# Kernel tuning notes

Measured on AMD Instinct MI355X. Metric: run time of the kernel, lower is better.

The kernel has to match this reference:

```python
import jax, jax.numpy as jnp
import numpy as np

B, S, DIM, NHEADS = 2, 3072, 1536, 12
HEAD_DIM = DIM // NHEADS          # 128
C = HEAD_DIM // 2                 # 64, freq channels per position
GRID = (8, 16, 24)                # F,H,W with F*H*W == S (static per this config)
EPS = 1e-6
MAX_POS = 1024


def _rms(x, g):
    # RMSNorm over the full channel dim (applied BEFORE per-head reshape, as in Wan)
    y = jax.lax.rsqrt(jnp.mean(jnp.square(x), axis=-1, keepdims=True) + EPS)
    return x * y * g


def _rope_angles(freqs, grid):
    # Split the C freq channels over (F, H, W) axes: [C-2*(C//3), C//3, C//3]
    s1 = C // 3
    s0 = C - 2 * s1
    f, h, w = grid
    af = freqs[:f, :s0]                # [f, s0]
    ah = freqs[:h, s0:s0 + s1]         # [h, s1]
    aw = freqs[:w, s0 + s1:]           # [w, s1]
    ang = jnp.concatenate([
        jnp.broadcast_to(af[:, None, None, :], (f, h, w, s0)),
        jnp.broadcast_to(ah[None, :, None, :], (f, h, w, s1)),
        jnp.broadcast_to(aw[None, None, :, :], (f, h, w, s1)),
    ], axis=-1)
    return ang.reshape(f * h * w, 1, C)  # [S, 1, C]


def _rope(x, ang):
    # x: [B, S, N, D]; rotate interleaved (even, odd) pairs by angle (complex mult)
    b, s, n, d = x.shape
    xr = x.reshape(b, s, n, d // 2, 2)
    cos = jnp.cos(ang)[None]           # [1, S, 1, C]
    sin = jnp.sin(ang)[None]
    ye = xr[..., 0] * cos - xr[..., 1] * sin
    yo = xr[..., 0] * sin + xr[..., 1] * cos
    return jnp.stack([ye, yo], axis=-1).reshape(b, s, n, d)


def setup_inputs() -> dict:
    key = jax.random.key(0)
    ks = jax.random.split(key, 12)
    x = jax.random.normal(ks[0], (B, S, DIM), dtype=jnp.float32)
    seq_lens = jnp.full((B,), S, dtype=jnp.int32)
    grid_sizes = np.array([list(GRID)] * B, dtype=np.int32)
    # Rotary angles: pos * inv_freq per channel (precomputed table, as in Wan)
    inv = 1.0 / (10000.0 ** (np.arange(C, dtype=np.float32) / C))
    freqs = jnp.asarray(np.arange(MAX_POS, dtype=np.float32)[:, None] * inv[None, :])
    w = lambda k: jax.random.normal(k, (DIM, DIM), dtype=jnp.float32) * 0.02
    bz = lambda: jnp.zeros((DIM,), dtype=jnp.float32)
    return {
        "x": x, "seq_lens": seq_lens, "grid_sizes": grid_sizes, "freqs": freqs,
        "Wq": w(ks[1]), "bq": bz(), "Wk": w(ks[2]), "bk": bz(),
        "Wv": w(ks[3]), "bv": bz(), "Wo": w(ks[4]), "bo": bz(),
        "gq": jnp.ones((DIM,), dtype=jnp.float32),
        "gk": jnp.ones((DIM,), dtype=jnp.float32),
    }


def reference(x, seq_lens, grid_sizes, freqs, Wq, bq, Wk, bk, Wv, bv, Wo, bo, gq, gk):
    b, s, _ = x.shape
    # QKV projection + full-dim RMSNorm on q/k
    q = _rms(x @ Wq.T + bq, gq).reshape(b, s, NHEADS, HEAD_DIM)
    k = _rms(x @ Wk.T + bk, gk).reshape(b, s, NHEADS, HEAD_DIM)
    v = (x @ Wv.T + bv).reshape(b, s, NHEADS, HEAD_DIM)
    # 3D RoPE (grid is static; all samples share GRID)
    ang = _rope_angles(freqs, GRID)
    q = _rope(q, ang)
    k = _rope(k, ang)
    # full (non-causal) attention with key-length masking
    scale = 1.0 / np.sqrt(HEAD_DIM).astype(np.float32)
    scores = jnp.einsum('bsnd,btnd->bnst', q, k) * scale
    kmask = jnp.arange(s)[None, :] < seq_lens[:, None]          # [B, T]
    scores = jnp.where(kmask[:, None, None, :], scores, jnp.float32(-1e30))
    attn = jax.nn.softmax(scores, axis=-1)
    out = jnp.einsum('bnst,btnd->bsnd', attn, v).reshape(b, s, DIM)
    return out @ Wo.T + bo
```

## Files before the change

### kernel.cpp

```cpp
#include <hip/hip_runtime.h>
#include <hip/hip_bf16.h>
#include <stdint.h>

typedef __attribute__((ext_vector_type(8))) short short8;
typedef __attribute__((ext_vector_type(4))) float f32x4;
typedef __attribute__((ext_vector_type(16))) float f32x16;

constexpr int kDim   = 1536;
constexpr int kHeads = 12;
constexpr int kHd    = 128;
constexpr int kS     = 3072;
constexpr int kB     = 2;
constexpr int kQKV   = 3 * kDim;
constexpr float kEps   = 1e-6f;
constexpr float kQMul  = 0.08838834764831845f * 1.44269504089f;

__device__ __forceinline__ ushort f2bf(float f) {
    union { float f; uint32_t u; } c; c.f = f;
    uint32_t u = c.u;
    return (ushort)((u + 0x7fffu + ((u >> 16) & 1u)) >> 16);
}
__device__ __forceinline__ float bf2f(uint32_t h) {
    union { uint32_t u; float f; } c; c.u = h << 16;
    return c.f;
}
__device__ __forceinline__ void gload_lds16(const void* g, void* l) {
    __builtin_amdgcn_global_load_lds((const __attribute__((address_space(1))) void*)g,
                                     (__attribute__((address_space(3))) void*)l, 16, 0, 0);
}
__device__ __forceinline__ uint32_t cvtpk_bf16(float lo, float hi) {
    uint32_t r;
    asm("v_cvt_pk_bf16_f32 %0, %1, %2" : "=v"(r) : "v"(lo), "v"(hi));
    return r;
}

__global__ __launch_bounds__(256)
void cvt_kernel(const float* __restrict__ in, ushort* __restrict__ out, int n8)
{
    int i = blockIdx.x * 256 + threadIdx.x;
    if (i >= n8) return;
    const float4* p = (const float4*)in + (size_t)i * 2;
    float4 a = p[0], b = p[1];
    uint4 r;
    r.x = (uint32_t)f2bf(a.x) | ((uint32_t)f2bf(a.y) << 16);
    r.y = (uint32_t)f2bf(a.z) | ((uint32_t)f2bf(a.w) << 16);
    r.z = (uint32_t)f2bf(b.x) | ((uint32_t)f2bf(b.y) << 16);
    r.w = (uint32_t)f2bf(b.z) | ((uint32_t)f2bf(b.w) << 16);
    ((uint4*)out)[i] = r;
}

__global__ __launch_bounds__(256)
void cvt4_kernel(const float* __restrict__ s0, const float* __restrict__ s1,
                 const float* __restrict__ s2, const float* __restrict__ s3,
                 ushort* __restrict__ d0, ushort* __restrict__ d1,
                 ushort* __restrict__ d2, ushort* __restrict__ d3, int n8)
{
    int i = blockIdx.x * 256 + threadIdx.x;
    if (i >= n8) return;
    const float* in; ushort* out;
    switch (blockIdx.y) {
        case 0: in = s0; out = d0; break;
        case 1: in = s1; out = d1; break;
        case 2: in = s2; out = d2; break;
        default: in = s3; out = d3; break;
    }
    const float4* p = (const float4*)in + (size_t)i * 2;
    float4 a = p[0], b = p[1];
    uint4 r;
    r.x = (uint32_t)f2bf(a.x) | ((uint32_t)f2bf(a.y) << 16);
    r.y = (uint32_t)f2bf(a.z) | ((uint32_t)f2bf(a.w) << 16);
    r.z = (uint32_t)f2bf(b.x) | ((uint32_t)f2bf(b.y) << 16);
    r.w = (uint32_t)f2bf(b.z) | ((uint32_t)f2bf(b.w) << 16);
    ((uint4*)out)[i] = r;
}

__global__ __launch_bounds__(256)
void biascat_kernel(const float* __restrict__ bq, const float* __restrict__ bk,
                    const float* __restrict__ bv, float* __restrict__ out)
{
    int i = blockIdx.x * 256 + threadIdx.x;
    if (i >= kQKV) return;
    float v = (i < kDim) ? bq[i] : (i < 2*kDim) ? bk[i - kDim] : bv[i - 2*kDim];
    out[i] = v;
}

template<typename OutT>
__global__ __launch_bounds__(256)
void gemm_bf16(const ushort* __restrict__ A, const ushort* __restrict__ B,
               const float* __restrict__ bias, OutT* __restrict__ C,
               int M, int N, int K)
{
    __shared__ ushort As[128 * 32];
    __shared__ ushort Bs[128 * 32];
    const int t    = threadIdx.x;
    const int lane = t & 63;
    const int w    = t >> 6;
    const int wm = (w >> 1) * 64, wn = (w & 1) * 64;
    const int m0 = blockIdx.y * 128, n0 = blockIdx.x * 128;

    const int srow = t >> 2;
    const int skc  = (t & 3) * 8;
    const ushort* Ag = A + (size_t)(m0 + srow) * K + skc;
    const ushort* Bg = B + (size_t)(n0 + srow) * K + skc;
    const size_t half = (size_t)64 * K;

    f32x4 acc[4][4];
    #pragma unroll
    for (int m = 0; m < 4; ++m)
        #pragma unroll
        for (int n = 0; n < 4; ++n)
            #pragma unroll
            for (int i = 0; i < 4; ++i) acc[m][n][i] = 0.f;

    const int kk  = (lane >> 4) * 8;
    const int l15 = lane & 15;

    for (int k0 = 0; k0 < K; k0 += 32) {
        __syncthreads();
        gload_lds16(Ag + k0,        &As[t * 8]);
        gload_lds16(Ag + half + k0, &As[t * 8 + 2048]);
        gload_lds16(Bg + k0,        &Bs[t * 8]);
        gload_lds16(Bg + half + k0, &Bs[t * 8 + 2048]);
        __syncthreads();
        short8 af[4], bf[4];
        #pragma unroll
        for (int m = 0; m < 4; ++m) af[m] = *(const short8*)&As[(wm + m*16 + l15) * 32 + kk];
        #pragma unroll
        for (int n = 0; n < 4; ++n) bf[n] = *(const short8*)&Bs[(wn + n*16 + l15) * 32 + kk];
        #pragma unroll
        for (int m = 0; m < 4; ++m)
            #pragma unroll
            for (int n = 0; n < 4; ++n)
                acc[m][n] = __builtin_amdgcn_mfma_f32_16x16x32_bf16(af[m], bf[n], acc[m][n], 0, 0, 0);
    }

    const int r0 = (lane >> 4) * 4;
    #pragma unroll
    for (int m = 0; m < 4; ++m) {
        #pragma unroll
        for (int r = 0; r < 4; ++r) {
            const size_t row = (size_t)(m0 + wm + m*16 + r0 + r);
            #pragma unroll
            for (int n = 0; n < 4; ++n) {
                const int col = n0 + wn + n*16 + l15;
                float val = acc[m][n][r] + bias[col];
                if constexpr (sizeof(OutT) == 4) C[row * N + col] = val;
                else                             C[row * N + col] = f2bf(val);
            }
        }
    }
}

__global__ __launch_bounds__(256)
void vtrans_kernel(const ushort* __restrict__ qkv, ushort* __restrict__ vt)
{
    __shared__ ushort Ts[64][72];
    const int t  = threadIdx.x;
    const int s0 = blockIdx.x * 64;
    const int d0 = blockIdx.y * 64;
    const int bh = blockIdx.z;
    const int b = bh / kHeads, h = bh % kHeads;

    const int r = t >> 2, cc = (t & 3) * 16;
    const ushort* src = qkv + ((size_t)(b * kS) + s0 + r) * kQKV + 2*kDim + h * kHd + d0 + cc;
    uint4 a0 = *(const uint4*)src;
    uint4 a1 = *(const uint4*)(src + 8);
    *(uint4*)&Ts[r][cc]     = a0;
    *(uint4*)&Ts[r][cc + 8] = a1;
    __syncthreads();
    ushort tmp[16];
    #pragma unroll
    for (int j = 0; j < 16; ++j) tmp[j] = Ts[cc + j][r];
    ushort* dst = vt + ((size_t)(bh * kHd) + d0 + r) * kS + s0 + cc;
    *(uint4*)dst       = *(uint4*)&tmp[0];
    *(uint4*)(dst + 8) = *(uint4*)&tmp[8];
}

__global__ __launch_bounds__(192)
void rmsrope_kernel(ushort* __restrict__ qkv,
                    const float* __restrict__ gq, const float* __restrict__ gk,
                    const float* __restrict__ freqs, const int* __restrict__ grid_sizes)
{
    __shared__ float red[4];
    const int row   = blockIdx.x;
    const int which = blockIdx.y;
    ushort* ptr = qkv + (size_t)row * kQKV + which * kDim;
    const float* g = which ? gk : gq;
    const float outmul = which ? 1.0f : kQMul;
    const int t = threadIdx.x;

    uint4 raw = ((const uint4*)ptr)[t];
    float v[8];
    v[0] = bf2f(raw.x & 0xffff); v[1] = bf2f(raw.x >> 16);
    v[2] = bf2f(raw.y & 0xffff); v[3] = bf2f(raw.y >> 16);
    v[4] = bf2f(raw.z & 0xffff); v[5] = bf2f(raw.z >> 16);
    v[6] = bf2f(raw.w & 0xffff); v[7] = bf2f(raw.w >> 16);

    float ss = 0.f;
    #pragma unroll
    for (int i = 0; i < 8; ++i) ss += v[i] * v[i];
    #pragma unroll
    for (int off = 32; off >= 1; off >>= 1) ss += __shfl_xor(ss, off);
    if ((t & 63) == 0) red[t >> 6] = ss;
    __syncthreads();
    const float scale = rsqrtf((red[0] + red[1] + red[2]) * (1.f / kDim) + kEps);

    const int b = row / kS, s = row % kS;
    const int gh = grid_sizes[b*3 + 1], gw = grid_sizes[b*3 + 2];
    const int hw  = gh * gw;
    const int fi  = s / hw;
    const int rem = s - fi * hw;
    const int hi  = rem / gw;
    const int wi  = rem - hi * gw;

    const float4 g0 = *(const float4*)(g + t*8);
    const float4 g1 = *(const float4*)(g + t*8 + 4);
    const float gv[8] = {g0.x, g0.y, g0.z, g0.w, g1.x, g1.y, g1.z, g1.w};

    uint32_t out[4];
    #pragma unroll
    for (int jj = 0; jj < 4; ++jj) {
        const int p = t*4 + jj;
        const int c = p & 63;
        const int pos = (c < 22) ? fi : (c < 43 ? hi : wi);
        const float ang = freqs[pos * 64 + c];
        float sn, cs;
        sincosf(ang, &sn, &cs);
        const float e0 = v[2*jj]   * scale * gv[2*jj];
        const float e1 = v[2*jj+1] * scale * gv[2*jj+1];
        const float o0 = (e0 * cs - e1 * sn) * outmul;
        const float o1 = (e0 * sn + e1 * cs) * outmul;
        out[jj] = (uint32_t)f2bf(o0) | ((uint32_t)f2bf(o1) << 16);
    }
    uint4 ov; ov.x = out[0]; ov.y = out[1]; ov.z = out[2]; ov.w = out[3];
    ((uint4*)ptr)[t] = ov;
}

__global__ __launch_bounds__(256, 2)
void attn_kernel(const ushort* __restrict__ qkv, const ushort* __restrict__ vtb,
                 ushort* __restrict__ pA, ushort* __restrict__ pB,
                 float* __restrict__ ml, const int* __restrict__ seq_lens)
{
    __shared__ ushort Ks[64 * 128];
    __shared__ ushort VT[128 * 64];

    const int lin = blockIdx.x;
    const int L   = (lin & 7) * 144 + (lin >> 3);
    const int bh   = L / 48;
    const int rem  = L - bh * 48;
    const int half = rem / 24;
    const int qtile= rem - half * 24;
    const int h = bh % kHeads, b = bh / kHeads;
    const int seq = seq_lens[b];
    const int kbeg = half * (kS / 2);

    const int t = threadIdx.x, lane = t & 63, w = t >> 6;
    const int l31 = lane & 31, hi = lane >> 5;
    const int qrow = qtile * 128 + w * 32 + l31;

    const ushort* qbase = qkv + ((size_t)b * kS) * kQKV + h * kHd;
    const ushort* kbase = qkv + ((size_t)b * kS) * kQKV + kDim + h * kHd;
    const ushort* vtbase = vtb + ((size_t)(b * kHeads + h) * kHd) * kS;

    short8 qf[8];
    #pragma unroll
    for (int kb = 0; kb < 8; ++kb)
        qf[kb] = *(const short8*)(qbase + (size_t)qrow * kQKV + kb*16 + hi*8);

    f32x16 oacc[4];
    #pragma unroll
    for (int n = 0; n < 4; ++n)
        #pragma unroll
        for (int i = 0; i < 16; ++i) oacc[n][i] = 0.f;

    float m_run = -1e30f, l_run = 0.f;

    const int srow = t >> 4;
    const int scol = (t & 15) * 8;
    const int kl   = scol ^ ((srow & 7) << 3);
    const int vd0  = t >> 3;
    const int vscol = ((t & 7) * 8) ^ ((vd0 & 7) << 3);

    for (int kt = 0; kt < kS/2; kt += 64) {
        const int k0 = kbeg + kt;
        __syncthreads();
        #pragma unroll
        for (int c = 0; c < 4; ++c) {
            gload_lds16(kbase + (size_t)(k0 + srow + c*16) * kQKV + kl, &Ks[t*8 + c*2048]);
            gload_lds16(vtbase + (size_t)(vd0 + c*32) * kS + k0 + vscol, &VT[t*8 + c*2048]);
        }
        __syncthreads();

        f32x16 s0, s1;
        #pragma unroll
        for (int i = 0; i < 16; ++i) { s0[i] = 0.f; s1[i] = 0.f; }
        __builtin_amdgcn_s_setprio(1);
        #pragma unroll
        for (int kb = 0; kb < 8; ++kb) {
            const int col = (kb*16 + hi*8) ^ ((l31 & 7) << 3);
            short8 kf0 = *(const short8*)&Ks[l31 * 128 + col];
            short8 kf1 = *(const short8*)&Ks[(32 + l31) * 128 + col];
            s0 = __builtin_amdgcn_mfma_f32_32x32x16_bf16(kf0, qf[kb], s0, 0, 0, 0);
            s1 = __builtin_amdgcn_mfma_f32_32x32x16_bf16(kf1, qf[kb], s1, 0, 0, 0);
        }
        __builtin_amdgcn_s_setprio(0);

        float mx = -1e30f;
        if (k0 + 64 > seq) {
            #pragma unroll
            for (int r = 0; r < 16; ++r) {
                const int key = k0 + (r&3) + 8*(r>>2) + 4*hi;
                if (key >= seq)      s0[r] = -1e30f;
                if (key + 32 >= seq) s1[r] = -1e30f;
                mx = fmaxf(fmaxf(mx, s0[r]), s1[r]);
            }
        } else {
            #pragma unroll
            for (int r = 0; r < 16; ++r) mx = fmaxf(fmaxf(mx, s0[r]), s1[r]);
        }
        mx = fmaxf(mx, __shfl_xor(mx, 32));

        const bool skip = (mx <= m_run + 11.0f);
        if (!__all(skip)) {
            const float mnew = fmaxf(m_run, mx);
            const float alpha = exp2f(m_run - mnew);
            m_run = mnew;
            l_run *= alpha;
            #pragma unroll
            for (int r = 0; r < 16; ++r) {
                const float ar = __shfl(alpha, (r&3) + 8*(r>>2) + 4*hi);
                #pragma unroll
                for (int n = 0; n < 4; ++n) oacc[n][r] *= ar;
            }
        }

        float rs = 0.f;
        #pragma unroll
        for (int r = 0; r < 16; ++r) {
            s0[r] = exp2f(s0[r] - m_run);
            s1[r] = exp2f(s1[r] - m_run);
            rs += s0[r] + s1[r];
        }
        rs += __shfl_xor(rs, 32);
        l_run += rs;

        uint32_t u0[8], u1[8], w0[8], w1[8];
        #pragma unroll
        for (int i = 0; i < 8; ++i) {
            u0[i] = cvtpk_bf16(s0[2*i], s0[2*i+1]);
            u1[i] = cvtpk_bf16(s1[2*i], s1[2*i+1]);
        }
        #pragma unroll
        for (int i = 0; i < 8; ++i) {
            w0[i] = __shfl_xor(u0[i], 32);
            w1[i] = __shfl_xor(u1[i], 32);
        }
        union PF { uint32_t d[4]; short8 s8; };
        PF pa[4];
        pa[0].d[0] = hi ? w0[2] : u0[0];  pa[0].d[1] = hi ? w0[3] : u0[1];
        pa[0].d[2] = hi ? u0[2] : w0[0];  pa[0].d[3] = hi ? u0[3] : w0[1];
        pa[1].d[0] = hi ? w0[6] : u0[4];  pa[1].d[1] = hi ? w0[7] : u0[5];
        pa[1].d[2] = hi ? u0[6] : w0[4];  pa[1].d[3] = hi ? u0[7] : w0[5];
        pa[2].d[0] = hi ? w1[2] : u1[0];  pa[2].d[1] = hi ? w1[3] : u1[1];
        pa[2].d[2] = hi ? u1[2] : w1[0];  pa[2].d[3] = hi ? u1[3] : w1[1];
        pa[3].d[0] = hi ? w1[6] : u1[4];  pa[3].d[1] = hi ? w1[7] : u1[5];
        pa[3].d[2] = hi ? u1[6] : w1[4];  pa[3].d[3] = hi ? u1[7] : w1[5];

        __builtin_amdgcn_s_setprio(1);
        #pragma unroll
        for (int ks = 0; ks < 4; ++ks) {
            #pragma unroll
            for (int n = 0; n < 4; ++n) {
                const int d = n*32 + l31;
                const int colv = (ks*16 + hi*8) ^ ((l31 & 7) << 3);
                short8 vf = *(const short8*)&VT[d * 64 + colv];
                oacc[n] = __builtin_amdgcn_mfma_f32_32x32x16_bf16(pa[ks].s8, vf, oacc[n], 0, 0, 0);
            }
        }
        __builtin_amdgcn_s_setprio(0);
    }

    ushort* pOut = half ? pB : pA;
    const float linv = 1.f / l_run;
    #pragma unroll
    for (int r = 0; r < 16; ++r) {
        const int qr = (r&3) + 8*(r>>2) + 4*hi;
        const float lr = __shfl(linv, qr);
        const size_t row = (size_t)(b * kS) + qtile * 128 + w * 32 + qr;
        #pragma unroll
        for (int n = 0; n < 4; ++n)
            pOut[row * kDim + h * kHd + n*32 + l31] = f2bf(oacc[n][r] * lr);
    }
    if (lane < 32) {
        const int s = qtile * 128 + w * 32 + l31;
        const size_t idx = ((((size_t)(b * kHeads + h)) * 2 + half) * kS + s) * 2;
        ml[idx]     = m_run;
        ml[idx + 1] = l_run;
    }
}

__global__ __launch_bounds__(256)
void combine_kernel(const ushort* __restrict__ pA, const ushort* __restrict__ pB,
                    const float* __restrict__ ml, ushort* __restrict__ out, int n8)
{
    int i = blockIdx.x * 256 + threadIdx.x;
    if (i >= n8) return;
    const int row = i / 192;
    const int within = (i - row * 192) * 8;
    const int h = within >> 7;
    const int b = row / kS;
    const int s = row - b * kS;
    const size_t base = (((size_t)(b * kHeads + h)) * 2) * kS;
    const float m0 = ml[(base + s) * 2],        l0 = ml[(base + s) * 2 + 1];
    const float m1 = ml[(base + kS + s) * 2],   l1 = ml[(base + kS + s) * 2 + 1];
    const float m  = fmaxf(m0, m1);
    const float a0 = l0 * exp2f(m0 - m);
    const float a1 = l1 * exp2f(m1 - m);
    const float inv = 1.f / (a0 + a1);
    const float f0 = a0 * inv, f1 = a1 * inv;

    uint4 ua = ((const uint4*)pA)[i];
    uint4 ub = ((const uint4*)pB)[i];
    const uint32_t* da = (const uint32_t*)&ua;
    const uint32_t* db = (const uint32_t*)&ub;
    uint32_t rv[4];
    #pragma unroll
    for (int j = 0; j < 4; ++j) {
        float o0 = f0 * bf2f(da[j] & 0xffff) + f1 * bf2f(db[j] & 0xffff);
        float o1 = f0 * bf2f(da[j] >> 16)    + f1 * bf2f(db[j] >> 16);
        rv[j] = (uint32_t)f2bf(o0) | ((uint32_t)f2bf(o1) << 16);
    }
    uint4 r; r.x = rv[0]; r.y = rv[1]; r.z = rv[2]; r.w = rv[3];
    ((uint4*)out)[i] = r;
}

extern "C" void kernel_launch(void* const* d_in, const int* in_sizes, int n_in,
                              void* d_out, int out_size, void* d_ws, size_t ws_size,
                              hipStream_t stream)
{
    (void)in_sizes; (void)n_in; (void)out_size; (void)ws_size;
    const float* x          = (const float*)d_in[0];
    const int*   seq_lens   = (const int*)  d_in[1];
    const int*   grid_sizes = (const int*)  d_in[2];
    const float* freqs      = (const float*)d_in[3];
    const float* Wq = (const float*)d_in[4];
    const float* bq = (const float*)d_in[5];
    const float* Wk = (const float*)d_in[6];
    const float* bk = (const float*)d_in[7];
    const float* Wv = (const float*)d_in[8];
    const float* bv = (const float*)d_in[9];
    const float* Wo = (const float*)d_in[10];
    const float* bo = (const float*)d_in[11];
    const float* gq = (const float*)d_in[12];
    const float* gk = (const float*)d_in[13];
    float* out = (float*)d_out;

    const int M = kB * kS;
    const size_t szX = (size_t)M * kDim;
    const size_t szW = (size_t)kDim * kDim;

    ushort* xb   = (ushort*)d_ws;
    ushort* wqb  = xb   + szX;
    ushort* wkb  = wqb  + szW;
    ushort* wvb  = wkb  + szW;
    ushort* wob  = wvb  + szW;
    ushort* qkvb = wob  + szW;
    ushort* ab   = qkvb + 3*szX;
    ushort* vtb  = ab   + szX;
    ushort* pBuf = vtb  + szX;
    float*  biasqkv = (float*)(pBuf + szX);
    float*  ml   = biasqkv + kQKV;

    dim3 blk(256);
    cvt_kernel<<<dim3((int)(szX/8/256)), blk, 0, stream>>>(x, xb, (int)(szX/8));
    cvt4_kernel<<<dim3((int)(szW/8/256), 4), blk, 0, stream>>>(
        Wq, Wk, Wv, Wo, wqb, wkb, wvb, wob, (int)(szW/8));
    biascat_kernel<<<dim3(18), blk, 0, stream>>>(bq, bk, bv, biasqkv);

    gemm_bf16<ushort><<<dim3(kQKV/128, M/128), blk, 0, stream>>>(
        xb, wqb, biasqkv, qkvb, M, kQKV, kDim);

    rmsrope_kernel<<<dim3(M, 2), dim3(192), 0, stream>>>(qkvb, gq, gk, freqs, grid_sizes);
    vtrans_kernel<<<dim3(kS/64, 2, kB*kHeads), blk, 0, stream>>>(qkvb, vtb);

    attn_kernel<<<dim3(48 * kHeads * kB), blk, 0, stream>>>(
        qkvb, vtb, xb, pBuf, ml, seq_lens);
    combine_kernel<<<dim3((int)(szX/8/256)), blk, 0, stream>>>(
        xb, pBuf, ml, ab, (int)(szX/8));

    gemm_bf16<float><<<dim3(kDim/128, M/128), blk, 0, stream>>>(
        ab, wob, bo, out, M, kDim, kDim);
}
```

Baseline: 433.6 us.

## Double-buffer LDS tiles in bf16 GEMM with two-stage prefetch

The GEMM kernel now keeps two LDS buffers for the A and B tiles. It preloads the first two K-slices, then, after computing on one buffer, refills that buffer with slice j+2 while the other buffer is consumed. The goal is to hide global-to-LDS load latency behind MFMA work and to drop one barrier per K step. In exchange, LDS use doubles to 32KB per block, and correctness relies on the barrier draining the asynchronous LDS loads before the next buffer is read.

```diff
diff --git a/kernel.cpp b/kernel.cpp
--- a/kernel.cpp
+++ b/kernel.cpp
@@ -90,8 +90,8 @@
                const float* __restrict__ bias, OutT* __restrict__ C,
                int M, int N, int K)
 {
-    __shared__ ushort As[128 * 32];
-    __shared__ ushort Bs[128 * 32];
+    __shared__ ushort As[2][128 * 32];
+    __shared__ ushort Bs[2][128 * 32];
     const int t    = threadIdx.x;
     const int lane = t & 63;
     const int w    = t >> 6;
@@ -103,6 +103,7 @@
     const ushort* Ag = A + (size_t)(m0 + srow) * K + skc;
     const ushort* Bg = B + (size_t)(n0 + srow) * K + skc;
     const size_t half = (size_t)64 * K;
+    const int Nk = K / 32;
 
     f32x4 acc[4][4];
     #pragma unroll
@@ -115,23 +116,39 @@
     const int kk  = (lane >> 4) * 8;
     const int l15 = lane & 15;
 
-    for (int k0 = 0; k0 < K; k0 += 32) {
-        __syncthreads();
-        gload_lds16(Ag + k0,        &As[t * 8]);
-        gload_lds16(Ag + half + k0, &As[t * 8 + 2048]);
-        gload_lds16(Bg + k0,        &Bs[t * 8]);
-        gload_lds16(Bg + half + k0, &Bs[t * 8 + 2048]);
-        __syncthreads();
+    {
+        gload_lds16(Ag,            &As[0][t * 8]);
+        gload_lds16(Ag + half,     &As[0][t * 8 + 2048]);
+        gload_lds16(Bg,            &Bs[0][t * 8]);
+        gload_lds16(Bg + half,     &Bs[0][t * 8 + 2048]);
+        gload_lds16(Ag + 32,        &As[1][t * 8]);
+        gload_lds16(Ag + half + 32, &As[1][t * 8 + 2048]);
+        gload_lds16(Bg + 32,        &Bs[1][t * 8]);
+        gload_lds16(Bg + half + 32, &Bs[1][t * 8 + 2048]);
+    }
+    __syncthreads();
+
+    for (int j = 0; j < Nk; ++j) {
+        const int cur = j & 1;
         short8 af[4], bf[4];
         #pragma unroll
-        for (int m = 0; m < 4; ++m) af[m] = *(const short8*)&As[(wm + m*16 + l15) * 32 + kk];
-        #pragma unroll
-        for (int n = 0; n < 4; ++n) bf[n] = *(const short8*)&Bs[(wn + n*16 + l15) * 32 + kk];
+        for (int m = 0; m < 4; ++m) af[m] = *(const short8*)&As[cur][(wm + m*16 + l15) * 32 + kk];
+        #pragma unroll
+        for (int n = 0; n < 4; ++n) bf[n] = *(const short8*)&Bs[cur][(wn + n*16 + l15) * 32 + kk];
         #pragma unroll
         for (int m = 0; m < 4; ++m)
             #pragma unroll
             for (int n = 0; n < 4; ++n)
                 acc[m][n] = __builtin_amdgcn_mfma_f32_16x16x32_bf16(af[m], bf[n], acc[m][n], 0, 0, 0);
+
+        __syncthreads();
+        if (j + 2 < Nk) {
+            const int k2 = (j + 2) * 32;
+            gload_lds16(Ag + k2,        &As[cur][t * 8]);
+            gload_lds16(Ag + half + k2, &As[cur][t * 8 + 2048]);
+            gload_lds16(Bg + k2,        &Bs[cur][t * 8]);
+            gload_lds16(Bg + half + k2, &Bs[cur][t * 8 + 2048]);
+        }
     }
 
     const int r0 = (lane >> 4) * 4;
```

Measured after the change: 439.2 us. Within noise of the previous version (+1.3%).

## Split attention key tile into two 32-key halves to cut registers, raise occupancy

Applied to the files above, without the earlier changes.

The 64-key inner step is restructured into two sequential 32-key sub-steps, each doing QK^T, online softmax update and PV for its half, so only one 16-float score accumulator and half the P fragments are live at once. Launch bounds are raised from 2 to 3 blocks per SIMD-group target so the compiler aims for lower VGPR use and more resident waves. The trade-off is twice as many max/rescale/shuffle reductions per tile and shorter MFMA chains between softmax phases. Spills are possible if the new register budget is too tight.

```diff
diff --git a/kernel.cpp b/kernel.cpp
--- a/kernel.cpp
+++ b/kernel.cpp
@@ -236,7 +236,7 @@
     ((uint4*)ptr)[t] = ov;
 }
 
-__global__ __launch_bounds__(256, 2)
+__global__ __launch_bounds__(256, 3)
 void attn_kernel(const ushort* __restrict__ qkv, const ushort* __restrict__ vtb,
                  ushort* __restrict__ pA, ushort* __restrict__ pB,
                  float* __restrict__ ml, const int* __restrict__ seq_lens)
@@ -291,93 +291,84 @@
         }
         __syncthreads();
 
-        f32x16 s0, s1;
-        #pragma unroll
-        for (int i = 0; i < 16; ++i) { s0[i] = 0.f; s1[i] = 0.f; }
-        __builtin_amdgcn_s_setprio(1);
-        #pragma unroll
-        for (int kb = 0; kb < 8; ++kb) {
-            const int col = (kb*16 + hi*8) ^ ((l31 & 7) << 3);
-            short8 kf0 = *(const short8*)&Ks[l31 * 128 + col];
-            short8 kf1 = *(const short8*)&Ks[(32 + l31) * 128 + col];
-            s0 = __builtin_amdgcn_mfma_f32_32x32x16_bf16(kf0, qf[kb], s0, 0, 0, 0);
-            s1 = __builtin_amdgcn_mfma_f32_32x32x16_bf16(kf1, qf[kb], s1, 0, 0, 0);
+        #pragma unroll
+        for (int hb = 0; hb < 2; ++hb) {
+            f32x16 s;
+            #pragma unroll
+            for (int i = 0; i < 16; ++i) s[i] = 0.f;
+            __builtin_amdgcn_s_setprio(1);
+            #pragma unroll
+            for (int kb = 0; kb < 8; ++kb) {
+                const int col = (kb*16 + hi*8) ^ ((l31 & 7) << 3);
+                short8 kf = *(const short8*)&Ks[(hb*32 + l31) * 128 + col];
+                s = __builtin_amdgcn_mfma_f32_32x32x16_bf16(kf, qf[kb], s, 0, 0, 0);
+            }
+            __builtin_amdgcn_s_setprio(0);
+
+            const int kb0 = k0 + hb*32;
+            float mx = -1e30f;
+            if (kb0 + 32 > seq) {
+                #pragma unroll
+                for (int r = 0; r < 16; ++r) {
+                    if (kb0 + (r&3) + 8*(r>>2) + 4*hi >= seq) s[r] = -1e30f;
+                    mx = fmaxf(mx, s[r]);
+                }
+            } else {
+                #pragma unroll
+                for (int r = 0; r < 16; ++r) mx = fmaxf(mx, s[r]);
+            }
+            mx = fmaxf(mx, __shfl_xor(mx, 32));
+
+            const bool skip = (mx <= m_run + 11.0f);
+            if (!__all(skip)) {
+                const float mnew = fmaxf(m_run, mx);
+                const float alpha = exp2f(m_run - mnew);
+                m_run = mnew;
+                l_run *= alpha;
+                #pragma unroll
+                for (int r = 0; r < 16; ++r) {
+                    const float ar = __shfl(alpha, (r&3) + 8*(r>>2) + 4*hi);
+                    #pragma unroll
+                    for (int n = 0; n < 4; ++n) oacc[n][r] *= ar;
+                }
+            }
+
+            float rs = 0.f;
+            #pragma unroll
+            for (int r = 0; r < 16; ++r) {
+                s[r] = exp2f(s[r] - m_run);
+                rs += s[r];
+            }
+            rs += __shfl_xor(rs, 32);
+            l_run += rs;
+
+            uint32_t u[8], wv[8];
+            #pragma unroll
+            for (int i = 0; i < 8; ++i) u[i] = cvtpk_bf16(s[2*i], s[2*i+1]);
+            #pragma unroll
+            for (int i = 0; i < 8; ++i) wv[i] = __shfl_xor(u[i], 32);
+            union PF { uint32_t d[4]; short8 s8; };
+            PF pa0, pa1;
+            pa0.d[0] = hi ? wv[2] : u[0];  pa0.d[1] = hi ? wv[3] : u[1];
+            pa0.d[2] = hi ? u[2] : wv[0];  pa0.d[3] = hi ? u[3] : wv[1];
+            pa1.d[0] = hi ? wv[6] : u[4];  pa1.d[1] = hi ? wv[7] : u[5];
+            pa1.d[2] = hi ? u[6] : wv[4];  pa1.d[3] = hi ? u[7] : wv[5];
+
+            __builtin_amdgcn_s_setprio(1);
+            #pragma unroll
+            for (int kss = 0; kss < 2; ++kss) {
+                const int ks = hb*2 + kss;
+                #pragma unroll
+                for (int n = 0; n < 4; ++n) {
+                    const int d = n*32 + l31;
+                    const int colv = (ks*16 + hi*8) ^ ((l31 & 7) << 3);
+                    short8 vf = *(const short8*)&VT[d * 64 + colv];
+                    oacc[n] = __builtin_amdgcn_mfma_f32_32x32x16_bf16(
+                        (kss ? pa1 : pa0).s8, vf, oacc[n], 0, 0, 0);
+                }
+            }
+            __builtin_amdgcn_s_setprio(0);
         }
-        __builtin_amdgcn_s_setprio(0);
-
-        float mx = -1e30f;
-        if (k0 + 64 > seq) {
-            #pragma unroll
-            for (int r = 0; r < 16; ++r) {
-                const int key = k0 + (r&3) + 8*(r>>2) + 4*hi;
-                if (key >= seq)      s0[r] = -1e30f;
-                if (key + 32 >= seq) s1[r] = -1e30f;
-                mx = fmaxf(fmaxf(mx, s0[r]), s1[r]);
-            }
-        } else {
-            #pragma unroll
-            for (int r = 0; r < 16; ++r) mx = fmaxf(fmaxf(mx, s0[r]), s1[r]);
-        }
-        mx = fmaxf(mx, __shfl_xor(mx, 32));
-
-        const bool skip = (mx <= m_run + 11.0f);
-        if (!__all(skip)) {
-            const float mnew = fmaxf(m_run, mx);
-            const float alpha = exp2f(m_run - mnew);
-            m_run = mnew;
-            l_run *= alpha;
-            #pragma unroll
-            for (int r = 0; r < 16; ++r) {
-                const float ar = __shfl(alpha, (r&3) + 8*(r>>2) + 4*hi);
-                #pragma unroll
-                for (int n = 0; n < 4; ++n) oacc[n][r] *= ar;
-            }
-        }
-
-        float rs = 0.f;
-        #pragma unroll
-        for (int r = 0; r < 16; ++r) {
-            s0[r] = exp2f(s0[r] - m_run);
-            s1[r] = exp2f(s1[r] - m_run);
-            rs += s0[r] + s1[r];
-        }
-        rs += __shfl_xor(rs, 32);
-        l_run += rs;
-
-        uint32_t u0[8], u1[8], w0[8], w1[8];
-        #pragma unroll
-        for (int i = 0; i < 8; ++i) {
-            u0[i] = cvtpk_bf16(s0[2*i], s0[2*i+1]);
-            u1[i] = cvtpk_bf16(s1[2*i], s1[2*i+1]);
-        }
-        #pragma unroll
-        for (int i = 0; i < 8; ++i) {
-            w0[i] = __shfl_xor(u0[i], 32);
-            w1[i] = __shfl_xor(u1[i], 32);
-        }
-        union PF { uint32_t d[4]; short8 s8; };
-        PF pa[4];
-        pa[0].d[0] = hi ? w0[2] : u0[0];  pa[0].d[1] = hi ? w0[3] : u0[1];
-        pa[0].d[2] = hi ? u0[2] : w0[0];  pa[0].d[3] = hi ? u0[3] : w0[1];
-        pa[1].d[0] = hi ? w0[6] : u0[4];  pa[1].d[1] = hi ? w0[7] : u0[5];
-        pa[1].d[2] = hi ? u0[6] : w0[4];  pa[1].d[3] = hi ? u0[7] : w0[5];
-        pa[2].d[0] = hi ? w1[2] : u1[0];  pa[2].d[1] = hi ? w1[3] : u1[1];
-        pa[2].d[2] = hi ? u1[2] : w1[0];  pa[2].d[3] = hi ? u1[3] : w1[1];
-        pa[3].d[0] = hi ? w1[6] : u1[4];  pa[3].d[1] = hi ? w1[7] : u1[5];
-        pa[3].d[2] = hi ? u1[6] : w1[4];  pa[3].d[3] = hi ? u1[7] : w1[5];
-
-        __builtin_amdgcn_s_setprio(1);
-        #pragma unroll
-        for (int ks = 0; ks < 4; ++ks) {
-            #pragma unroll
-            for (int n = 0; n < 4; ++n) {
-                const int d = n*32 + l31;
-                const int colv = (ks*16 + hi*8) ^ ((l31 & 7) << 3);
-                short8 vf = *(const short8*)&VT[d * 64 + colv];
-                oacc[n] = __builtin_amdgcn_mfma_f32_32x32x16_bf16(pa[ks].s8, vf, oacc[n], 0, 0, 0);
-            }
-        }
-        __builtin_amdgcn_s_setprio(0);
     }
 
     ushort* pOut = half ? pB : pA;
```

New measurement: 421.8 us (median of 2 runs). 1.03x faster.
